# Kernel tuning notes

Measured on AMD Instinct MI355X. Metric: run time of the kernel, lower is better.

Reference implementation:

```python
import jax, jax.numpy as jnp
import numpy as np

B, H, L, DK = 8, 8, 512, 64
LK, C = 512, 5


def setup_inputs() -> dict:
    key = jax.random.key(0)
    ks = jax.random.split(key, 6)
    d_in = LK * H * DK  # l_k * d_model
    return {
        "Q": jax.random.normal(ks[0], (B, H, L, DK), dtype=jnp.float32),
        "K": jax.random.normal(ks[1], (B, H, LK, DK), dtype=jnp.float32),
        # scale by 1/sqrt(fan_in) so softmax inputs are sane
        "W_proj": jax.random.normal(ks[2], (d_in, C), dtype=jnp.float32) / np.sqrt(d_in),
        "b_proj": jnp.zeros((C,), dtype=jnp.float32),
        "W_q": jax.random.normal(ks[3], (C, C), dtype=jnp.float32) / np.sqrt(C),
        "b_q": jnp.zeros((C,), dtype=jnp.float32),
        "W_k": jax.random.normal(ks[4], (C, C), dtype=jnp.float32) / np.sqrt(C),
        "b_k": jnp.zeros((C,), dtype=jnp.float32),
    }


def reference(Q, K, W_proj, b_proj, W_q, b_q, W_k, b_k):
    b, h, l, d_k = Q.shape
    l_k = K.shape[2]
    n_clusters = b_proj.shape[0]
    hd = h * d_k

    # cluster projections over flattened K
    ck_proj = K.reshape(b, -1) @ W_proj + b_proj            # (b, C)
    cluster_q = jax.nn.softmax(ck_proj @ W_q + b_q, axis=-1)  # (b, C)
    cluster_k = jax.nn.softmax(ck_proj @ W_k + b_k, axis=-1)  # (b, C)

    # Gaussian likelihood term (torch.std is unbiased -> ddof=1)
    mu = jnp.mean(cluster_q, axis=0)                         # (C,)
    sigma = jax.nn.softplus(jnp.std(cluster_k, axis=0, ddof=1))
    log_prob = (-0.5 * ((cluster_k - mu) / sigma) ** 2
                - jnp.log(sigma) - 0.5 * jnp.log(2.0 * jnp.pi))
    # CrossEntropyLoss with prob targets: mean_b(-sum target*log_softmax(input))
    ce = jnp.mean(-jnp.sum(cluster_q * jax.nn.log_softmax(cluster_q, axis=-1), axis=-1))
    loss = -jnp.mean(log_prob) + ce

    # cluster assignment per batch element
    inds = jnp.argmax(cluster_q, axis=-1)                    # (b,) in [0, C)

    # The original per-cluster loop with where(K_cluster != i+1, K_inds, 0) then
    # mean(dim=0)[0] reduces to: mean over batch of K_re[:,0,:] masked where
    # assignment != i+1, broadcast across l_k.
    K_re = K.reshape(b, l_k, hd)
    row0 = K_re[:, 0, :]                                     # (b, hd)
    keep = (inds[None, :] != (jnp.arange(n_clusters) + 1)[:, None]).astype(Q.dtype)  # (C, b)
    means = (keep @ row0) / b                                # (C, hd)

    # broadcast to (b, C, l_k, hd) then raw reshape to (b, h, C, l_k, d_k)
    cm = jnp.broadcast_to(means[None, :, None, :], (b, n_clusters, l_k, hd))
    cm = cm.reshape(b, h, n_clusters, l_k, d_k)

    scale = 1.0 / np.sqrt(d_k)
    scores_qk = jnp.einsum('bhqd,bhkd->bhqk', Q, K) * scale          # (b,h,l,l_k)
    scores_qc = jnp.einsum('bhqd,bhckd->bhcqk', Q, cm) * scale       # (b,h,C,l,l_k)
    # max over cat([qk, qc], dim=2) == elementwise max of qk and max_c qc
    final_score = jnp.maximum(scores_qk, jnp.max(scores_qc, axis=2))
    return final_score, loss
```

## Files before the change

kernel.cpp:

```cpp
#include <hip/hip_runtime.h>
#include <math.h>

#define NB 8
#define NH 8
#define SEQ 512
#define DK 64
#define NC 5
#define D_IN 262144
#define OUT_SCORE (NB*NH*SEQ*SEQ)
#define PROJ_BLOCKS 128

typedef short short8 __attribute__((ext_vector_type(8)));
typedef float f32x16 __attribute__((ext_vector_type(16)));

__device__ __forceinline__ short f2bf(float f) {
  unsigned u = __float_as_uint(f);
  u += 0x7fffu + ((u >> 16) & 1u);
  return (short)(u >> 16);
}
__device__ __forceinline__ short8 pack8(float4 a, float4 b) {
  short8 r;
  r[0] = f2bf(a.x); r[1] = f2bf(a.y); r[2] = f2bf(a.z); r[3] = f2bf(a.w);
  r[4] = f2bf(b.x); r[5] = f2bf(b.y); r[6] = f2bf(b.z); r[7] = f2bf(b.w);
  return r;
}

__global__ __launch_bounds__(256) void proj_kernel(const float* __restrict__ K,
                                                   const float* __restrict__ Wp,
                                                   float* __restrict__ part) {
  const float4* Wp4 = (const float4*)Wp;
  float acc[NB][NC];
#pragma unroll
  for (int b = 0; b < NB; ++b)
#pragma unroll
    for (int c = 0; c < NC; ++c) acc[b][c] = 0.f;

#pragma unroll
  for (int it = 0; it < 2; ++it) {
    int i4 = blockIdx.x * 512 + it * 256 + threadIdx.x;
    float w[20];
#pragma unroll
    for (int t = 0; t < 5; ++t) {
      float4 v = Wp4[i4 * 5 + t];
      w[4*t+0] = v.x; w[4*t+1] = v.y; w[4*t+2] = v.z; w[4*t+3] = v.w;
    }
#pragma unroll
    for (int b = 0; b < NB; ++b) {
      float4 kv = ((const float4*)(K + (size_t)b * D_IN))[i4];
      float ke[4] = {kv.x, kv.y, kv.z, kv.w};
#pragma unroll
      for (int e = 0; e < 4; ++e)
#pragma unroll
        for (int c = 0; c < NC; ++c)
          acc[b][c] = fmaf(ke[e], w[5*e + c], acc[b][c]);
    }
  }

  __shared__ float red[4][NB * NC];
  int wave = threadIdx.x >> 6;
  int lane = threadIdx.x & 63;
#pragma unroll
  for (int bc = 0; bc < NB * NC; ++bc) {
    float v = acc[bc / NC][bc % NC];
#pragma unroll
    for (int off = 32; off > 0; off >>= 1) v += __shfl_down(v, off);
    if (lane == 0) red[wave][bc] = v;
  }
  __syncthreads();
  if (threadIdx.x < NB * NC)
    part[blockIdx.x * (NB * NC) + threadIdx.x] =
        red[0][threadIdx.x] + red[1][threadIdx.x] +
        red[2][threadIdx.x] + red[3][threadIdx.x];
}

__global__ __launch_bounds__(256) void small_kernel(
    const float* __restrict__ K, const float* __restrict__ part,
    const float* __restrict__ bp, const float* __restrict__ Wq,
    const float* __restrict__ bq, const float* __restrict__ Wk,
    const float* __restrict__ bk, float* __restrict__ means,
    float* __restrict__ loss_out) {
  __shared__ float colsum[NB * NC];
  __shared__ float cq[NB][NC], ckk[NB][NC], ce_sh[NB];
  __shared__ int inds[NB];
  int t = threadIdx.x;
  if (t < NB * NC) {
    float s = 0.f;
    for (int i = 0; i < PROJ_BLOCKS; ++i) s += part[i * (NB * NC) + t];
    colsum[t] = s;
  }
  __syncthreads();
  if (t < NB) {
    float cp[NC], zq[NC], zk[NC];
#pragma unroll
    for (int c = 0; c < NC; ++c) cp[c] = colsum[t * NC + c] + bp[c];
#pragma unroll
    for (int c = 0; c < NC; ++c) { zq[c] = bq[c]; zk[c] = bk[c]; }
#pragma unroll
    for (int j = 0; j < NC; ++j)
#pragma unroll
      for (int c = 0; c < NC; ++c) {
        zq[c] = fmaf(cp[j], Wq[j * NC + c], zq[c]);
        zk[c] = fmaf(cp[j], Wk[j * NC + c], zk[c]);
      }
    float m = zq[0];
#pragma unroll
    for (int c = 1; c < NC; ++c) m = fmaxf(m, zq[c]);
    float e[NC], s = 0.f;
#pragma unroll
    for (int c = 0; c < NC; ++c) { e[c] = expf(zq[c] - m); s += e[c]; }
    float inv = 1.f / s;
    float p[NC];
#pragma unroll
    for (int c = 0; c < NC; ++c) { p[c] = e[c] * inv; cq[t][c] = p[c]; }
    int am = 0; float bv = p[0];
#pragma unroll
    for (int c = 1; c < NC; ++c) if (p[c] > bv) { bv = p[c]; am = c; }
    inds[t] = am;
    float se = 0.f;
#pragma unroll
    for (int c = 0; c < NC; ++c) se += expf(p[c] - bv);
    float lse = bv + logf(se);
    float ceb = 0.f;
#pragma unroll
    for (int c = 0; c < NC; ++c) ceb -= p[c] * (p[c] - lse);
    ce_sh[t] = ceb;
    m = zk[0];
#pragma unroll
    for (int c = 1; c < NC; ++c) m = fmaxf(m, zk[c]);
    s = 0.f;
#pragma unroll
    for (int c = 0; c < NC; ++c) { e[c] = expf(zk[c] - m); s += e[c]; }
    inv = 1.f / s;
#pragma unroll
    for (int c = 0; c < NC; ++c) ckk[t][c] = e[c] * inv;
  }
  __syncthreads();
  if (t == 0) {
    float mu[NC];
#pragma unroll
    for (int c = 0; c < NC; ++c) {
      float sm = 0.f;
      for (int b = 0; b < NB; ++b) sm += cq[b][c];
      mu[c] = sm * 0.125f;
    }
    float loss_lp = 0.f;
#pragma unroll
    for (int c = 0; c < NC; ++c) {
      float sm = 0.f;
      for (int b = 0; b < NB; ++b) sm += ckk[b][c];
      float mk = sm * 0.125f;
      float var = 0.f;
      for (int b = 0; b < NB; ++b) {
        float d = ckk[b][c] - mk;
        var += d * d;
      }
      var *= (1.f / 7.f);
      float sd = sqrtf(var);
      float sigma = log1pf(expf(sd));
      float ls = logf(sigma);
      for (int b = 0; b < NB; ++b) {
        float z = (ckk[b][c] - mu[c]) / sigma;
        loss_lp += -0.5f * z * z - ls - 0.91893853320467274f;
      }
    }
    float ce = 0.f;
    for (int b = 0; b < NB; ++b) ce += ce_sh[b];
    ce *= 0.125f;
    loss_out[0] = -(loss_lp / 40.f) + ce;
  }
  __syncthreads();
  for (int idx = t; idx < NC * 512; idx += 256) {
    int c = idx >> 9, j = idx & 511;
    float sm = 0.f;
#pragma unroll
    for (int b = 0; b < NB; ++b)
      if (inds[b] != c + 1) sm += K[(size_t)b * D_IN + j];
    means[idx] = sm * 0.125f;
  }
}

#define LDSTRIDE 72
__global__ __launch_bounds__(256) void score_kernel(const float* __restrict__ Q,
                                                    const float* __restrict__ K,
                                                    const float* __restrict__ means,
                                                    float* __restrict__ out) {
  __shared__ short Qs[128 * LDSTRIDE];
  __shared__ short Ks[64 * LDSTRIDE];
  __shared__ float qcbuf[4 * 32 * 10];

  const int bh = blockIdx.x;
  const int h  = bh & 7;
  const int qblk = blockIdx.y << 7;
  const int kblk = blockIdx.z << 6;
  const int tid = threadIdx.x;
  const int w = tid >> 6, lane = tid & 63;
  const int lo5 = lane & 31, hi = lane >> 5;
  const int wq = w << 5;

  const float* Qg = Q + (size_t)bh * (SEQ * DK) + (size_t)qblk * DK;
  const float* Kg = K + (size_t)bh * (SEQ * DK) + (size_t)kblk * DK;

#pragma unroll
  for (int i = 0; i < 4; ++i) {
    int f8 = i * 256 + tid;
    int row = f8 >> 3, c8 = f8 & 7;
    const float4* qp = (const float4*)(Qg + row * DK + c8 * 8);
    *(short8*)&Qs[row * LDSTRIDE + c8 * 8] = pack8(qp[0], qp[1]);
  }
#pragma unroll
  for (int i = 0; i < 2; ++i) {
    int f8 = i * 256 + tid;
    int row = f8 >> 3, c8 = f8 & 7;
    const float4* kp = (const float4*)(Kg + row * DK + c8 * 8);
    *(short8*)&Ks[row * LDSTRIDE + c8 * 8] = pack8(kp[0], kp[1]);
  }

  const int cmin = (5 * h) >> 3;
  const int cmax = (5 * h + 4) >> 3;
  short8 mfrag[4];
#pragma unroll
  for (int s = 0; s < 4; ++s) {
    float4 a = {0.f, 0.f, 0.f, 0.f}, b = {0.f, 0.f, 0.f, 0.f};
    if (lo5 < 16) {
      int c = (lo5 < 8) ? cmin : cmax;
      const float* mp = means + c * 512 + (lo5 & 7) * 64 + s * 16 + hi * 8;
      a = *(const float4*)mp;
      b = *(const float4*)(mp + 4);
    }
    mfrag[s] = pack8(a, b);
  }

  __syncthreads();

  f32x16 zero;
#pragma unroll
  for (int x = 0; x < 16; ++x) zero[x] = 0.f;

  f32x16 acc0 = zero, acc1 = zero, aq = zero;
#pragma unroll
  for (int s = 0; s < 4; ++s) {
    int co = s * 16 + hi * 8;
    short8 a  = *(const short8*)&Qs[(wq + lo5)  * LDSTRIDE + co];
    short8 b0 = *(const short8*)&Ks[lo5         * LDSTRIDE + co];
    short8 b1 = *(const short8*)&Ks[(32 + lo5)  * LDSTRIDE + co];
    acc0 = __builtin_amdgcn_mfma_f32_32x32x16_bf16(a, b0, acc0, 0, 0, 0);
    acc1 = __builtin_amdgcn_mfma_f32_32x32x16_bf16(a, b1, acc1, 0, 0, 0);
    aq   = __builtin_amdgcn_mfma_f32_32x32x16_bf16(mfrag[s], a, aq, 0, 0, 0);
  }

  {
    int qb = w * 320 + lo5 * 10 + 4 * hi;
    float2 p;
    p.x = fmaxf(aq[0], aq[4]) * 0.125f;
    p.y = fmaxf(aq[1], aq[5]) * 0.125f;
    *(float2*)&qcbuf[qb] = p;
    p.x = fmaxf(aq[2], aq[6]) * 0.125f;
    p.y = fmaxf(aq[3], aq[7]) * 0.125f;
    *(float2*)&qcbuf[qb + 2] = p;
  }

  float* ob = out + (size_t)bh * (SEQ * SEQ);
  const int kc0 = kblk + lo5;
  const int r = lo5 & 7;
  const int qcb = w * 320 + r;
#pragma unroll
  for (int g = 0; g < 4; ++g) {
#pragma unroll
    for (int e = 0; e < 4; ++e) {
      int reg = 4 * g + e;
      int ql = e + 8 * g + 4 * hi;
      float qc = qcbuf[qcb + ql * 10];
      int qrow = qblk + wq + ql;
      ob[(size_t)qrow * SEQ + kc0]      = fmaxf(acc0[reg] * 0.125f, qc);
      ob[(size_t)qrow * SEQ + kc0 + 32] = fmaxf(acc1[reg] * 0.125f, qc);
    }
  }
}

extern "C" void kernel_launch(void* const* d_in, const int* in_sizes, int n_in,
                              void* d_out, int out_size, void* d_ws, size_t ws_size,
                              hipStream_t stream) {
  const float* Q  = (const float*)d_in[0];
  const float* K  = (const float*)d_in[1];
  const float* Wp = (const float*)d_in[2];
  const float* bp = (const float*)d_in[3];
  const float* Wq = (const float*)d_in[4];
  const float* bq = (const float*)d_in[5];
  const float* Wk = (const float*)d_in[6];
  const float* bk = (const float*)d_in[7];
  float* out = (float*)d_out;

  float* part  = (float*)d_ws;
  float* means = part + PROJ_BLOCKS * NB * NC;

  proj_kernel<<<PROJ_BLOCKS, 256, 0, stream>>>(K, Wp, part);
  small_kernel<<<1, 256, 0, stream>>>(K, part, bp, Wq, bq, Wk, bk, means,
                                      out + OUT_SCORE);
  dim3 grid(64, 4, 8);
  score_kernel<<<grid, 256, 0, stream>>>(Q, K, means, out);
}
```

Baseline: 133.3 us.

## Fuse projection and small reduction kernels via cooperative grid sync; nontemporal score stores

Merges the projection partial-sum kernel and the single-block loss/means kernel into one cooperative launch that uses a grid-wide barrier, which removes one kernel launch and its gap. The final column sum is split across 160 threads instead of 40. The score kernel now writes its output with nontemporal stores to avoid cache pollution on the large streaming write. Cooperative launch adds its own grid-sync and launch overhead, which could offset the saved launch.

```diff
diff --git a/kernel.cpp b/kernel.cpp
--- a/kernel.cpp
+++ b/kernel.cpp
@@ -1,5 +1,8 @@
 #include <hip/hip_runtime.h>
+#include <hip/hip_cooperative_groups.h>
 #include <math.h>
+
+namespace cg = cooperative_groups;
 
 #define NB 8
 #define NH 8
@@ -25,9 +28,12 @@
   return r;
 }
 
-__global__ __launch_bounds__(256) void proj_kernel(const float* __restrict__ K,
-                                                   const float* __restrict__ Wp,
-                                                   float* __restrict__ part) {
+__global__ __launch_bounds__(256) void proj_small_kernel(
+    const float* __restrict__ K, const float* __restrict__ Wp,
+    float* __restrict__ part, const float* __restrict__ bp,
+    const float* __restrict__ Wq, const float* __restrict__ bq,
+    const float* __restrict__ Wk, const float* __restrict__ bk,
+    float* __restrict__ means, float* __restrict__ loss_out) {
   const float4* Wp4 = (const float4*)Wp;
   float acc[NB][NC];
 #pragma unroll
@@ -57,38 +63,47 @@
   }
 
   __shared__ float red[4][NB * NC];
-  int wave = threadIdx.x >> 6;
-  int lane = threadIdx.x & 63;
-#pragma unroll
-  for (int bc = 0; bc < NB * NC; ++bc) {
-    float v = acc[bc / NC][bc % NC];
-#pragma unroll
-    for (int off = 32; off > 0; off >>= 1) v += __shfl_down(v, off);
-    if (lane == 0) red[wave][bc] = v;
-  }
-  __syncthreads();
-  if (threadIdx.x < NB * NC)
-    part[blockIdx.x * (NB * NC) + threadIdx.x] =
-        red[0][threadIdx.x] + red[1][threadIdx.x] +
-        red[2][threadIdx.x] + red[3][threadIdx.x];
-}
-
-__global__ __launch_bounds__(256) void small_kernel(
-    const float* __restrict__ K, const float* __restrict__ part,
-    const float* __restrict__ bp, const float* __restrict__ Wq,
-    const float* __restrict__ bq, const float* __restrict__ Wk,
-    const float* __restrict__ bk, float* __restrict__ means,
-    float* __restrict__ loss_out) {
+  {
+    int wave = threadIdx.x >> 6;
+    int lane = threadIdx.x & 63;
+#pragma unroll
+    for (int bc = 0; bc < NB * NC; ++bc) {
+      float v = acc[bc / NC][bc % NC];
+#pragma unroll
+      for (int off = 32; off > 0; off >>= 1) v += __shfl_down(v, off);
+      if (lane == 0) red[wave][bc] = v;
+    }
+    __syncthreads();
+    if (threadIdx.x < NB * NC)
+      part[blockIdx.x * (NB * NC) + threadIdx.x] =
+          red[0][threadIdx.x] + red[1][threadIdx.x] +
+          red[2][threadIdx.x] + red[3][threadIdx.x];
+  }
+
+  __threadfence();
+  cg::this_grid().sync();
+
+  if (blockIdx.x != 0) return;
+
+  __shared__ float cs4[4][NB * NC];
   __shared__ float colsum[NB * NC];
   __shared__ float cq[NB][NC], ckk[NB][NC], ce_sh[NB];
   __shared__ int inds[NB];
   int t = threadIdx.x;
-  if (t < NB * NC) {
+
+  if (t < 160) {
+    int sl = t / 40;
+    int c  = t - sl * 40;
     float s = 0.f;
-    for (int i = 0; i < PROJ_BLOCKS; ++i) s += part[i * (NB * NC) + t];
-    colsum[t] = s;
-  }
-  __syncthreads();
+#pragma unroll
+    for (int i = 0; i < 32; ++i) s += part[(sl * 32 + i) * (NB * NC) + c];
+    cs4[sl][c] = s;
+  }
+  __syncthreads();
+  if (t < NB * NC)
+    colsum[t] = cs4[0][t] + cs4[1][t] + cs4[2][t] + cs4[3][t];
+  __syncthreads();
+
   if (t < NB) {
     float cp[NC], zq[NC], zk[NC];
 #pragma unroll
@@ -271,8 +286,10 @@
       int ql = e + 8 * g + 4 * hi;
       float qc = qcbuf[qcb + ql * 10];
       int qrow = qblk + wq + ql;
-      ob[(size_t)qrow * SEQ + kc0]      = fmaxf(acc0[reg] * 0.125f, qc);
-      ob[(size_t)qrow * SEQ + kc0 + 32] = fmaxf(acc1[reg] * 0.125f, qc);
+      __builtin_nontemporal_store(fmaxf(acc0[reg] * 0.125f, qc),
+                                  &ob[(size_t)qrow * SEQ + kc0]);
+      __builtin_nontemporal_store(fmaxf(acc1[reg] * 0.125f, qc),
+                                  &ob[(size_t)qrow * SEQ + kc0 + 32]);
     }
   }
 }
@@ -292,10 +309,14 @@
 
   float* part  = (float*)d_ws;
   float* means = part + PROJ_BLOCKS * NB * NC;
-
-  proj_kernel<<<PROJ_BLOCKS, 256, 0, stream>>>(K, Wp, part);
-  small_kernel<<<1, 256, 0, stream>>>(K, part, bp, Wq, bq, Wk, bk, means,
-                                      out + OUT_SCORE);
+  float* loss_out = out + OUT_SCORE;
+
+  void* args[] = {(void*)&K,  (void*)&Wp, (void*)&part, (void*)&bp,
+                  (void*)&Wq, (void*)&bq, (void*)&Wk,   (void*)&bk,
+                  (void*)&means, (void*)&loss_out};
+  hipLaunchCooperativeKernel((const void*)proj_small_kernel,
+                             dim3(PROJ_BLOCKS), dim3(256), args, 0, stream);
+
   dim3 grid(64, 4, 8);
   score_kernel<<<grid, 256, 0, stream>>>(Q, K, means, out);
 }
```

Measured after the change: 173.6 us. 30.2% more time.

## Swizzle score grid for XCD locality, use nontemporal stores, parallelize partial reduction

Applied to the files above, without the earlier changes.

The score kernel moves to a flat 2048-block grid and remaps block IDs so that consecutive blocks on the same XCD (blockIdx mod 8) cover the same batch-head and query tile, which should improve L2 reuse of Q and K. Output stores become nontemporal so the 8M-float score write does not pollute the cache. The small kernel spreads the 128-way partial-sum reduction across 160 threads in four slices instead of 40 threads. The risk is that the swizzle mapping assumes round-robin XCD dispatch, and nontemporal stores could slow writes on some paths.

```diff
diff --git a/kernel.cpp b/kernel.cpp
--- a/kernel.cpp
+++ b/kernel.cpp
@@ -79,15 +79,22 @@
     const float* __restrict__ bq, const float* __restrict__ Wk,
     const float* __restrict__ bk, float* __restrict__ means,
     float* __restrict__ loss_out) {
+  __shared__ float cs4[4][NB * NC];
   __shared__ float colsum[NB * NC];
   __shared__ float cq[NB][NC], ckk[NB][NC], ce_sh[NB];
   __shared__ int inds[NB];
   int t = threadIdx.x;
-  if (t < NB * NC) {
+  if (t < 160) {
+    int sl = t / 40;
+    int c  = t - sl * 40;
     float s = 0.f;
-    for (int i = 0; i < PROJ_BLOCKS; ++i) s += part[i * (NB * NC) + t];
-    colsum[t] = s;
-  }
+#pragma unroll
+    for (int i = 0; i < 32; ++i) s += part[(sl * 32 + i) * (NB * NC) + c];
+    cs4[sl][c] = s;
+  }
+  __syncthreads();
+  if (t < NB * NC)
+    colsum[t] = cs4[0][t] + cs4[1][t] + cs4[2][t] + cs4[3][t];
   __syncthreads();
   if (t < NB) {
     float cp[NC], zq[NC], zk[NC];
@@ -188,10 +195,12 @@
   __shared__ short Ks[64 * LDSTRIDE];
   __shared__ float qcbuf[4 * 32 * 10];
 
-  const int bh = blockIdx.x;
+  const int swz = (blockIdx.x & 7) * 256 + (blockIdx.x >> 3);
+  const int kblk = (swz & 7) << 6;
+  const int grp  = swz >> 3;
+  const int qblk = (grp & 3) << 7;
+  const int bh   = grp >> 2;
   const int h  = bh & 7;
-  const int qblk = blockIdx.y << 7;
-  const int kblk = blockIdx.z << 6;
   const int tid = threadIdx.x;
   const int w = tid >> 6, lane = tid & 63;
   const int lo5 = lane & 31, hi = lane >> 5;
@@ -271,8 +280,10 @@
       int ql = e + 8 * g + 4 * hi;
       float qc = qcbuf[qcb + ql * 10];
       int qrow = qblk + wq + ql;
-      ob[(size_t)qrow * SEQ + kc0]      = fmaxf(acc0[reg] * 0.125f, qc);
-      ob[(size_t)qrow * SEQ + kc0 + 32] = fmaxf(acc1[reg] * 0.125f, qc);
+      __builtin_nontemporal_store(fmaxf(acc0[reg] * 0.125f, qc),
+                                  &ob[(size_t)qrow * SEQ + kc0]);
+      __builtin_nontemporal_store(fmaxf(acc1[reg] * 0.125f, qc),
+                                  &ob[(size_t)qrow * SEQ + kc0 + 32]);
     }
   }
 }
@@ -296,6 +307,5 @@
   proj_kernel<<<PROJ_BLOCKS, 256, 0, stream>>>(K, Wp, part);
   small_kernel<<<1, 256, 0, stream>>>(K, part, bp, Wq, bq, Wk, bk, means,
                                       out + OUT_SCORE);
-  dim3 grid(64, 4, 8);
-  score_kernel<<<grid, 256, 0, stream>>>(Q, K, means, out);
-}
+  score_kernel<<<2048, 256, 0, stream>>>(Q, K, means, out);
+}
```

New measurement: 138.0 us. 1.04x slower.
